# Kernel optimization log

Hardware: AMD Instinct MI355X
Metric: run time of the kernel (lower is better)

The kernel has to match this reference:

```python
import jax, jax.numpy as jnp
import numpy as np

D_MODEL = 1024
NUM_HEADS = 16
HEAD_DIM = D_MODEL // NUM_HEADS
B, T = 4, 2048


def setup_inputs() -> dict:
    key = jax.random.key(0)
    ks = jax.random.split(key, 10)
    s = 1.0 / np.sqrt(D_MODEL)
    inp = {
        'x': jax.random.normal(ks[0], (B, T, D_MODEL), dtype=jnp.float32),
        'padding_mask': jnp.zeros((B, T), dtype=bool),
        'Wq': jax.random.uniform(ks[1], (D_MODEL, D_MODEL), minval=-s, maxval=s),
        'bq': jax.random.uniform(ks[2], (D_MODEL,), minval=-s, maxval=s),
        'Wk': jax.random.uniform(ks[3], (D_MODEL, D_MODEL), minval=-s, maxval=s),
        'bk': jax.random.uniform(ks[4], (D_MODEL,), minval=-s, maxval=s),
        'Wv': jax.random.uniform(ks[5], (D_MODEL, D_MODEL), minval=-s, maxval=s),
        'bv': jax.random.uniform(ks[6], (D_MODEL,), minval=-s, maxval=s),
        'Wo': jax.random.uniform(ks[7], (D_MODEL, D_MODEL), minval=-s, maxval=s),
        'bo': jax.random.uniform(ks[8], (D_MODEL,), minval=-s, maxval=s),
    }
    return inp


def reference(x, padding_mask, Wq, bq, Wk, bk, Wv, bv, Wo, bo):
    Bx, Tx, Dx = x.shape
    # projections (nn.Linear: x @ W^T + b)
    q = (x @ Wq.T + bq).reshape(Bx, Tx, NUM_HEADS, HEAD_DIM).transpose(0, 2, 1, 3)
    k = (x @ Wk.T + bk).reshape(Bx, Tx, NUM_HEADS, HEAD_DIM).transpose(0, 2, 1, 3)
    v = (x @ Wv.T + bv).reshape(Bx, Tx, NUM_HEADS, HEAD_DIM).transpose(0, 2, 1, 3)
    scale = jnp.sqrt(jnp.asarray(HEAD_DIM, dtype=x.dtype))
    attn = jnp.einsum('bhqd,bhkd->bhqk', q, k) / scale  # (B,H,T,T)
    causal = jnp.triu(jnp.ones((Tx, Tx), dtype=bool), k=1)
    neg_inf = jnp.asarray(-jnp.inf, dtype=attn.dtype)
    attn = jnp.where(causal[None, None], neg_inf, attn)
    attn = jnp.where(padding_mask[:, None, None, :], neg_inf, attn)
    attn = jax.nn.softmax(attn, axis=-1)
    # dropout is identity in eval / p=0.0
    out = jnp.einsum('bhqk,bhkd->bhqd', attn, v)
    out = out.transpose(0, 2, 1, 3).reshape(Bx, Tx, Dx)
    return out @ Wo.T + bo
```

## Files before the change

### kernel.cpp

```cpp
#include <hip/hip_runtime.h>

typedef __bf16 bf16x8 __attribute__((ext_vector_type(8)));
typedef float  f32x4  __attribute__((ext_vector_type(4)));
typedef unsigned short u16;
typedef u16 u16x8 __attribute__((ext_vector_type(8)));

#define MFMA16(a, b, c) __builtin_amdgcn_mfma_f32_16x16x32_bf16((a), (b), (c), 0, 0, 0)

__device__ __forceinline__ u16 f2bf(float f) {
    union { float f; unsigned u; } x; x.f = f;
    unsigned r = x.u + 0x7fffu + ((x.u >> 16) & 1u);
    return (u16)(r >> 16);
}

__device__ __forceinline__ void gll16(const void* g, void* l) {
    __builtin_amdgcn_global_load_lds(
        (const __attribute__((address_space(1))) void*)g,
        (__attribute__((address_space(3))) void*)l, 16, 0, 0);
}

#define QSCL 0.18033688f

__global__ __launch_bounds__(256) void cvt5_kernel(const float* __restrict__ x,
                                                   const float* __restrict__ wq,
                                                   const float* __restrict__ wk,
                                                   const float* __restrict__ wv,
                                                   const float* __restrict__ wo,
                                                   u16* __restrict__ xb,
                                                   u16* __restrict__ wqkvb,
                                                   u16* __restrict__ wob) {
    const int i = blockIdx.x * 256 + threadIdx.x;
    const float* src;
    u16* dst;
    int off;
    if (i < 2097152) {
        src = x; dst = xb; off = i;
    } else {
        const int jj = i - 2097152;
        const int sel = jj >> 18;
        off = jj & 262143;
        if (sel == 0)      { src = wq; dst = wqkvb; }
        else if (sel == 1) { src = wk; dst = wqkvb + 1024 * 1024; }
        else if (sel == 2) { src = wv; dst = wqkvb + 2 * 1024 * 1024; }
        else               { src = wo; dst = wob; }
    }
    float4 v = ((const float4*)src)[off];
    ushort4 o;
    o.x = f2bf(v.x); o.y = f2bf(v.y); o.z = f2bf(v.z); o.w = f2bf(v.w);
    ((ushort4*)dst)[off] = o;
}

__global__ __launch_bounds__(256) void vtrans_kernel(const u16* __restrict__ v,
                                                     u16* __restrict__ vt) {
    __shared__ u16 Ls[64][72];
    const int bh = blockIdx.y;
    const int jt = blockIdx.x;
    const int tid = threadIdx.x;
    const u16* src = v + ((size_t)bh * 2048 + jt * 64) * 64;
#pragma unroll
    for (int p = 0; p < 2; p++) {
        int idx = p * 256 + tid;
        int r = idx >> 3, c0 = (idx & 7) * 8;
        *(u16x8*)&Ls[r][c0] = *(const u16x8*)(src + r * 64 + c0);
    }
    __syncthreads();
    u16* dst = vt + (size_t)bh * 64 * 2048 + jt * 64;
#pragma unroll
    for (int p = 0; p < 2; p++) {
        int idx = p * 256 + tid;
        int d = idx >> 3, t0 = (idx & 7) * 8;
        u16x8 o;
#pragma unroll
        for (int i = 0; i < 8; i++) o[i] = Ls[t0 + i][d];
        *(u16x8*)(dst + (size_t)d * 2048 + t0) = o;
    }
}

template <int MODE>
__global__ __launch_bounds__(256) void gemm_bt(const u16* __restrict__ A,
                                               const u16* __restrict__ Bm,
                                               const float* __restrict__ b0,
                                               const float* __restrict__ b1,
                                               const float* __restrict__ b2,
                                               u16* __restrict__ qo,
                                               u16* __restrict__ ko,
                                               u16* __restrict__ vo,
                                               float* __restrict__ outp) {
    __shared__ u16 As[128 * 32];
    __shared__ u16 Bs[128 * 32];
    const int tid = threadIdx.x;
    const int w = tid >> 6, l = tid & 63;
    const int wr = w >> 1, wc = w & 1;
    const int lr = l & 15, lg = l >> 4;
    const int m0 = blockIdx.y * 128, n0 = blockIdx.x * 128;

    f32x4 acc[4][4];
#pragma unroll
    for (int i = 0; i < 4; i++)
#pragma unroll
        for (int j = 0; j < 4; j++) acc[i][j] = (f32x4){0.f, 0.f, 0.f, 0.f};

    const int srow = tid >> 2;
    const int scol = (tid & 3) * 8;

    for (int kk0 = 0; kk0 < 1024; kk0 += 32) {
        const u16* ag = A + (size_t)(m0 + srow) * 1024 + kk0 + scol;
        gll16(ag, As + tid * 8);
        gll16(ag + (size_t)64 * 1024, As + 2048 + tid * 8);
        const u16* bg = Bm + (size_t)(n0 + srow) * 1024 + kk0 + scol;
        gll16(bg, Bs + tid * 8);
        gll16(bg + (size_t)64 * 1024, Bs + 2048 + tid * 8);
        __syncthreads();

        bf16x8 af[4], bfb[4];
#pragma unroll
        for (int mi = 0; mi < 4; mi++)
            af[mi] = *(const bf16x8*)&As[(wr * 64 + mi * 16 + lr) * 32 + lg * 8];
#pragma unroll
        for (int ni = 0; ni < 4; ni++)
            bfb[ni] = *(const bf16x8*)&Bs[(wc * 64 + ni * 16 + lr) * 32 + lg * 8];
#pragma unroll
        for (int mi = 0; mi < 4; mi++)
#pragma unroll
            for (int ni = 0; ni < 4; ni++)
                acc[mi][ni] = MFMA16(af[mi], bfb[ni], acc[mi][ni]);
        __syncthreads();
    }

#pragma unroll
    for (int mi = 0; mi < 4; mi++) {
#pragma unroll
        for (int ni = 0; ni < 4; ni++) {
            const int ng = n0 + wc * 64 + ni * 16 + lr;
#pragma unroll
            for (int jj = 0; jj < 4; jj++) {
                const int mg = m0 + wr * 64 + mi * 16 + lg * 4 + jj;
                float val = acc[mi][ni][jj];
                if (MODE == 0) {
                    const int which = ng >> 10;
                    const int nn = ng & 1023;
                    const float* bsel = (which == 0) ? b0 : (which == 1) ? b1 : b2;
                    val += bsel[nn];
                    if (which == 0) val *= QSCL;
                    const int hh = nn >> 6, dc = nn & 63;
                    const int bb = mg >> 11, tt = mg & 2047;
                    u16* dst = (which == 0) ? qo : (which == 1) ? ko : vo;
                    dst[(((size_t)(bb * 16 + hh)) * 2048 + tt) * 64 + dc] = f2bf(val);
                } else {
                    val += b0[ng];
                    outp[(size_t)mg * 1024 + ng] = val;
                }
            }
        }
    }
}

__global__ __launch_bounds__(512) void attn_kernel(const u16* __restrict__ q,
                                                   const u16* __restrict__ k,
                                                   const u16* __restrict__ vt,
                                                   u16* __restrict__ ao) {
    __shared__ u16 Ks[2][4096];
    __shared__ u16 Vs[2][4096];
    __shared__ u16 Ps[8][1024];

    const int idx = blockIdx.x;
    const int j = idx & 63;
    const int bh = ((j & 7) << 3) | (j >> 3);
    const int qt = idx >> 6;
    const int b = bh >> 4, h = bh & 15;
    const int tid = threadIdx.x;
    const int w = tid >> 6, l = tid & 63;
    const int lr = l & 15, lg = l >> 4;

    const u16* qb = q + (size_t)bh * 2048 * 64;
    const u16* kb = k + (size_t)bh * 2048 * 64;
    const u16* vtb = vt + (size_t)bh * 64 * 2048;

    const int r0 = qt * 128 + w * 16;

    bf16x8 qf[2];
    {
        const int row = r0 + lr;
        qf[0] = *(const bf16x8*)(qb + (size_t)row * 64 + lg * 8);
        qf[1] = *(const bf16x8*)(qb + (size_t)row * 64 + 32 + lg * 8);
    }

    const int u = tid;
    const int ke = (u * 8) ^ (((u >> 3) & 7) << 3);
    const int vd = u >> 3, vc = ((u & 7) * 8) ^ ((vd & 7) << 3);

    float m_[4], lsum[4];
    f32x4 acc[4];
#pragma unroll
    for (int jj = 0; jj < 4; jj++) {
        m_[jj] = -INFINITY; lsum[jj] = 0.f;
        acc[jj] = (f32x4){0.f, 0.f, 0.f, 0.f};
    }

    const int nt = 2 * qt + 2;

    gll16(kb + ke, &Ks[0][0] + u * 8);
    gll16(vtb + (size_t)vd * 2048 + vc, &Vs[0][0] + u * 8);

    int cur = 0;
    for (int jt = 0; jt < nt; ++jt) {
        __syncthreads();

        if (jt + 1 < nt) {
            const int nxt = cur ^ 1;
            gll16(kb + (size_t)(jt + 1) * 4096 + ke, &Ks[nxt][0] + u * 8);
            gll16(vtb + (size_t)vd * 2048 + (jt + 1) * 64 + vc, &Vs[nxt][0] + u * 8);
        }

        const int k0 = jt * 64;
        if (k0 <= r0 + 15) {
            f32x4 sf[4];
#pragma unroll
            for (int nb = 0; nb < 4; ++nb) {
                const int e0 = (nb * 16 + lr) * 64 + lg * 8;
                const int sx = (lr & 7) << 3;
                bf16x8 bk0 = *(const bf16x8*)&Ks[cur][e0 ^ sx];
                bf16x8 bk1 = *(const bf16x8*)&Ks[cur][(e0 + 32) ^ sx];
                f32x4 s = (f32x4){0.f, 0.f, 0.f, 0.f};
                s = MFMA16(qf[0], bk0, s);
                s = MFMA16(qf[1], bk1, s);
                sf[nb] = s;
            }

            const bool needmask = (k0 + 63 > r0);
            const int d0 = r0 + lg * 4 - k0 - lr;
#pragma unroll
            for (int jj = 0; jj < 4; jj++) {
                if (needmask) {
#pragma unroll
                    for (int nb = 0; nb < 4; nb++)
                        if (nb * 16 > d0 + jj) sf[nb][jj] = -INFINITY;
                }
                float mx = fmaxf(fmaxf(sf[0][jj], sf[1][jj]), fmaxf(sf[2][jj], sf[3][jj]));
#pragma unroll
                for (int d = 1; d < 16; d <<= 1) mx = fmaxf(mx, __shfl_xor(mx, d));
                const float mnew = fmaxf(m_[jj], mx);
                const float sc = __builtin_amdgcn_exp2f(m_[jj] - mnew);
                m_[jj] = mnew;
                lsum[jj] *= sc;
                acc[0][jj] *= sc; acc[1][jj] *= sc; acc[2][jj] *= sc; acc[3][jj] *= sc;
                float ps = 0.f;
#pragma unroll
                for (int nb = 0; nb < 4; nb++) {
                    float p = __builtin_amdgcn_exp2f(sf[nb][jj] - mnew);
                    sf[nb][jj] = p;
                    ps += p;
                }
                lsum[jj] += ps;
            }

            u16* Pw = &Ps[w][0];
            asm volatile("s_waitcnt lgkmcnt(0)" ::: "memory");
#pragma unroll
            for (int nb = 0; nb < 4; nb++)
#pragma unroll
                for (int jj = 0; jj < 4; jj++) {
                    const int row = lg * 4 + jj;
                    const int e = row * 64 + nb * 16 + lr;
                    Pw[e ^ ((row & 7) << 3)] = f2bf(sf[nb][jj]);
                }
            asm volatile("s_waitcnt lgkmcnt(0)" ::: "memory");
            __builtin_amdgcn_sched_barrier(0);

#pragma unroll
            for (int kb2 = 0; kb2 < 2; ++kb2) {
                const int ep = lr * 64 + kb2 * 32 + lg * 8;
                bf16x8 pa = *(const bf16x8*)&Pw[ep ^ ((lr & 7) << 3)];
#pragma unroll
                for (int nb = 0; nb < 4; nb++) {
                    const int ev = (nb * 16 + lr) * 64 + kb2 * 32 + lg * 8;
                    bf16x8 vf = *(const bf16x8*)&Vs[cur][ev ^ ((lr & 7) << 3)];
                    acc[nb] = MFMA16(pa, vf, acc[nb]);
                }
            }
        }
        cur ^= 1;
    }

    const int trow = r0 + lg * 4;
    u16* aob = ao + ((size_t)b * 2048) * 1024 + h * 64;
#pragma unroll
    for (int jj = 0; jj < 4; jj++) {
        float t = lsum[jj];
#pragma unroll
        for (int d = 1; d < 16; d <<= 1) t += __shfl_xor(t, d);
        const float inv = 1.0f / t;
#pragma unroll
        for (int nb = 0; nb < 4; nb++)
            aob[(size_t)(trow + jj) * 1024 + nb * 16 + lr] = f2bf(acc[nb][jj] * inv);
    }
}

extern "C" void kernel_launch(void* const* d_in, const int* in_sizes, int n_in,
                              void* d_out, int out_size, void* d_ws, size_t ws_size,
                              hipStream_t stream) {
    const float* x  = (const float*)d_in[0];
    const float* Wq = (const float*)d_in[2];
    const float* bq = (const float*)d_in[3];
    const float* Wk = (const float*)d_in[4];
    const float* bk = (const float*)d_in[5];
    const float* Wv = (const float*)d_in[6];
    const float* bv = (const float*)d_in[7];
    const float* Wo = (const float*)d_in[8];
    const float* bo = (const float*)d_in[9];
    float* out = (float*)d_out;

    const size_t MD = (size_t)8192 * 1024;
    u16* xb   = (u16*)d_ws;
    u16* wqkv = xb + MD;
    u16* wo   = wqkv + 3 * 1024 * 1024;
    u16* qw   = wo + 1024 * 1024;
    u16* kw   = qw + MD;
    u16* vw   = kw + MD;
    u16* vtw  = xb;
    u16* ao   = vw;

    cvt5_kernel<<<12288, 256, 0, stream>>>(x, Wq, Wk, Wv, Wo, xb, wqkv, wo);

    gemm_bt<0><<<dim3(24, 64), 256, 0, stream>>>(xb, wqkv, bq, bk, bv,
                                                 qw, kw, vw, nullptr);

    vtrans_kernel<<<dim3(32, 64), 256, 0, stream>>>(vw, vtw);

    attn_kernel<<<1024, 512, 0, stream>>>(qw, kw, vtw, ao);

    gemm_bt<1><<<dim3(8, 64), 256, 0, stream>>>(ao, wo, bo, bo, bo,
                                                nullptr, nullptr, nullptr, out);
}
```

Before: 227.0 us.

## Halve P staging buffer with two-phase P@V and skip rescale when max unchanged

The per-wave P tile in LDS shrinks to half size and is written and consumed in two 32-column halves, each followed by its P@V MFMAs. The goal is lower LDS footprint, which may help occupancy, and interleaving of P writes with MFMA work. Separately, the online-softmax rescale of the accumulators and row sums is skipped when no lane's row max increased, saving exp and multiply work. The trade is an extra LDS wait/barrier round per tile and a warp-wide vote branch.

```diff
diff --git a/kernel.cpp b/kernel.cpp
--- a/kernel.cpp
+++ b/kernel.cpp
@@ -161,7 +161,7 @@
                                                    u16* __restrict__ ao) {
     __shared__ u16 Ks[2][4096];
     __shared__ u16 Vs[2][4096];
-    __shared__ u16 Ps[8][1024];
+    __shared__ u16 Ps[8][512];
 
     const int idx = blockIdx.x;
     const int j = idx & 63;
@@ -239,15 +239,18 @@
                 float mx = fmaxf(fmaxf(sf[0][jj], sf[1][jj]), fmaxf(sf[2][jj], sf[3][jj]));
 #pragma unroll
                 for (int d = 1; d < 16; d <<= 1) mx = fmaxf(mx, __shfl_xor(mx, d));
-                const float mnew = fmaxf(m_[jj], mx);
-                const float sc = __builtin_amdgcn_exp2f(m_[jj] - mnew);
-                m_[jj] = mnew;
-                lsum[jj] *= sc;
-                acc[0][jj] *= sc; acc[1][jj] *= sc; acc[2][jj] *= sc; acc[3][jj] *= sc;
+                if (!__all(mx <= m_[jj])) {
+                    const float mnew = fmaxf(m_[jj], mx);
+                    const float sc = __builtin_amdgcn_exp2f(m_[jj] - mnew);
+                    m_[jj] = mnew;
+                    lsum[jj] *= sc;
+                    acc[0][jj] *= sc; acc[1][jj] *= sc;
+                    acc[2][jj] *= sc; acc[3][jj] *= sc;
+                }
                 float ps = 0.f;
 #pragma unroll
                 for (int nb = 0; nb < 4; nb++) {
-                    float p = __builtin_amdgcn_exp2f(sf[nb][jj] - mnew);
+                    float p = __builtin_amdgcn_exp2f(sf[nb][jj] - m_[jj]);
                     sf[nb][jj] = p;
                     ps += p;
                 }
@@ -255,25 +258,46 @@
             }
 
             u16* Pw = &Ps[w][0];
+
             asm volatile("s_waitcnt lgkmcnt(0)" ::: "memory");
 #pragma unroll
-            for (int nb = 0; nb < 4; nb++)
+            for (int nb = 0; nb < 2; nb++)
 #pragma unroll
                 for (int jj = 0; jj < 4; jj++) {
                     const int row = lg * 4 + jj;
-                    const int e = row * 64 + nb * 16 + lr;
-                    Pw[e ^ ((row & 7) << 3)] = f2bf(sf[nb][jj]);
+                    const int e = row * 32 + nb * 16 + lr;
+                    Pw[e ^ ((row & 3) << 3)] = f2bf(sf[nb][jj]);
                 }
             asm volatile("s_waitcnt lgkmcnt(0)" ::: "memory");
             __builtin_amdgcn_sched_barrier(0);
-
-#pragma unroll
-            for (int kb2 = 0; kb2 < 2; ++kb2) {
-                const int ep = lr * 64 + kb2 * 32 + lg * 8;
-                bf16x8 pa = *(const bf16x8*)&Pw[ep ^ ((lr & 7) << 3)];
+            {
+                const int ep = (lr * 32 + lg * 8) ^ ((lr & 3) << 3);
+                bf16x8 pa = *(const bf16x8*)&Pw[ep];
 #pragma unroll
                 for (int nb = 0; nb < 4; nb++) {
-                    const int ev = (nb * 16 + lr) * 64 + kb2 * 32 + lg * 8;
+                    const int ev = (nb * 16 + lr) * 64 + lg * 8;
+                    bf16x8 vf = *(const bf16x8*)&Vs[cur][ev ^ ((lr & 7) << 3)];
+                    acc[nb] = MFMA16(pa, vf, acc[nb]);
+                }
+            }
+
+            asm volatile("s_waitcnt lgkmcnt(0)" ::: "memory");
+#pragma unroll
+            for (int nb = 2; nb < 4; nb++)
+#pragma unroll
+                for (int jj = 0; jj < 4; jj++) {
+                    const int row = lg * 4 + jj;
+                    const int e = row * 32 + (nb - 2) * 16 + lr;
+                    Pw[e ^ ((row & 3) << 3)] = f2bf(sf[nb][jj]);
+                }
+            asm volatile("s_waitcnt lgkmcnt(0)" ::: "memory");
+            __builtin_amdgcn_sched_barrier(0);
+            {
+                const int ep = (lr * 32 + lg * 8) ^ ((lr & 3) << 3);
+                bf16x8 pa = *(const bf16x8*)&Pw[ep];
+#pragma unroll
+                for (int nb = 0; nb < 4; nb++) {
+                    const int ev = (nb * 16 + lr) * 64 + 32 + lg * 8;
                     bf16x8 vf = *(const bf16x8*)&Vs[cur][ev ^ ((lr & 7) << 3)];
                     acc[nb] = MFMA16(pa, vf, acc[nb]);
                 }
```

Result: slower. 240.3 us (+5.8%).
